# Optimization experiments

Measured on AMD Instinct MI355X. Metric: run time of the kernel, lower is better.

Reference implementation:

```python
import jax, jax.numpy as jnp
import numpy as np

N = 10000
E = 640000
D = 128
EPS = 1e-8


def _gcn_conv(x, src, dst, deg_isqrt, W, b, n):
    # PyG GCNConv: h = x @ W; out_i = sum_{j->i} (d_j^-1/2 d_i^-1/2) h_j; out += b
    h = x @ W                                   # [N, Dout]
    norm = deg_isqrt[src] * deg_isqrt[dst]      # [E']
    msgs = h[src] * norm[:, None]               # [E', Dout] gather
    out = jax.ops.segment_sum(msgs, dst, num_segments=n)  # scatter-add
    return out + b


def _pairnorm_pn(x):
    # mode 'PN': divide each row by its L2 norm
    norm = jnp.sqrt(jnp.sum(x * x, axis=1, keepdims=True)) + EPS
    return x / norm


def setup_inputs() -> dict:
    key = jax.random.key(0)
    ks = jax.random.split(key, 8)
    x = jax.random.normal(ks[0], (N, D), dtype=jnp.float32)
    edge_index = jax.random.randint(ks[1], (2, E), 0, N, dtype=jnp.int64)
    scale = 1.0 / np.sqrt(D)
    W1 = jax.random.normal(ks[2], (D, D), dtype=jnp.float32) * scale
    b1 = jnp.zeros((D,), dtype=jnp.float32)
    W2 = jax.random.normal(ks[3], (D, D), dtype=jnp.float32) * scale
    b2 = jnp.zeros((D,), dtype=jnp.float32)
    W3 = jax.random.normal(ks[4], (D, D), dtype=jnp.float32) * scale
    b3 = jnp.zeros((D,), dtype=jnp.float32)
    return {"x": x, "edge_index": edge_index, "W1": W1, "b1": b1,
            "W2": W2, "b2": b2, "W3": W3, "b3": b3}


def reference(x, edge_index, W1, b1, W2, b2, W3, b3):
    n = x.shape[0]
    loops = jnp.arange(n, dtype=edge_index.dtype)
    src = jnp.concatenate([edge_index[0], loops])  # add self loops
    dst = jnp.concatenate([edge_index[1], loops])
    deg = jax.ops.segment_sum(jnp.ones_like(dst, dtype=x.dtype), dst, num_segments=n)
    deg_isqrt = jnp.where(deg > 0, jax.lax.rsqrt(jnp.maximum(deg, 1.0)), 0.0)

    prev = x  # in_channels == hidden_channels -> identity skip
    for W, b in ((W1, b1), (W2, b2)):
        x = _gcn_conv(x, src, dst, deg_isqrt, W, b, n)
        x = _pairnorm_pn(x)
        x = x + prev
        prev = x
        x = jax.nn.gelu(x, approximate=False)  # torch F.gelu default = exact erf
        # dropout p=0.0 / eval: identity
    return _gcn_conv(x, src, dst, deg_isqrt, W3, b3, n)
```

## Files before the change

kernel.cpp:

```cpp
#include <hip/hip_runtime.h>
#include <hip/hip_bf16.h>
#include <hip/hip_fp16.h>
#include <math.h>

#define D 128
#define PAD 16
#define MAXDEG 192
#define WKROW 65

typedef _Float16 h2 __attribute__((ext_vector_type(2)));

__global__ void zero_strided(int* __restrict__ p, int n) {
    int i = blockIdx.x * blockDim.x + threadIdx.x;
    if (i < n) p[(size_t)i * PAD] = 0;
}

__global__ void csr_direct(const int* __restrict__ ei, int E,
                           int* __restrict__ cnt, unsigned short* __restrict__ slots) {
    int t = blockIdx.x * blockDim.x + threadIdx.x;
    int e0 = t * 2;
    if (e0 + 1 < E) {
        int2 s = *(const int2*)(ei + e0);
        int2 d = *(const int2*)(ei + E + e0);
        int p0 = atomicAdd(&cnt[(size_t)d.x * PAD], 1);
        int p1 = atomicAdd(&cnt[(size_t)d.y * PAD], 1);
        if (p0 < MAXDEG) __builtin_nontemporal_store((unsigned short)s.x, &slots[(size_t)d.x * MAXDEG + p0]);
        if (p1 < MAXDEG) __builtin_nontemporal_store((unsigned short)s.y, &slots[(size_t)d.y * MAXDEG + p1]);
    } else if (e0 < E) {
        int sv = ei[e0], dv = ei[E + e0];
        int p = atomicAdd(&cnt[(size_t)dv * PAD], 1);
        if (p < MAXDEG) __builtin_nontemporal_store((unsigned short)sv, &slots[(size_t)dv * MAXDEG + p]);
    }
}

__global__ void prep_kernel(const float* __restrict__ x, const int* __restrict__ cnt,
                            unsigned* __restrict__ xb, int n) {
    int t = blockIdx.x * blockDim.x + threadIdx.x;
    if (t < n * 64) {
        int i = t >> 6;
        float di = rsqrtf((float)(cnt[(size_t)i * PAD] + 1));
        float2 v = ((const float2*)x)[t];
        union { h2 h; unsigned u; } pk;
        pk.h = (h2){(_Float16)(di * v.x), (_Float16)(di * v.y)};
        xb[t] = pk.u;
    }
}

__device__ __forceinline__ h2 shxor_h2(h2 v, int m) {
    union { h2 h; int i; } a, b;
    a.h = v;
    b.i = __shfl_xor(a.i, m);
    return b.h;
}

union U4H { uint4 u; h2 h[4]; };

#define ACCH(U) do { ha0 += (U).h[0]; ha1 += (U).h[1]; ha2 += (U).h[2]; ha3 += (U).h[3]; } while (0)

__global__ __launch_bounds__(512, 8) void layer_kernel(
        const unsigned* __restrict__ xb,
        const int* __restrict__ cnt, const unsigned short* __restrict__ slots,
        const float* __restrict__ W, const float* __restrict__ bias,
        const float* __restrict__ prev, float* __restrict__ pout,
        unsigned* __restrict__ xbout, float* __restrict__ out3,
        int n, int mode, int wp) {
    __shared__ unsigned Wk[D * WKROW];
    __shared__ unsigned yh[8 * 64];
    {
        const float4* W4 = (const float4*)W;
#pragma unroll
        for (int it = 0; it < 4; ++it) {
            int t2 = it * 512 + threadIdx.x;
            int k2 = t2 >> 5, c4 = t2 & 31;
            float4 wa = W4[(2 * k2) * 32 + c4];
            float4 wb = W4[(2 * k2 + 1) * 32 + c4];
            int jb = c4 << 2;
            union { h2 h; unsigned u; } p0, p1, p2, p3;
            p0.h = (h2){(_Float16)wa.x, (_Float16)wb.x};
            p1.h = (h2){(_Float16)wa.y, (_Float16)wb.y};
            p2.h = (h2){(_Float16)wa.z, (_Float16)wb.z};
            p3.h = (h2){(_Float16)wa.w, (_Float16)wb.w};
            Wk[(jb + 0) * WKROW + k2] = p0.u;
            Wk[(jb + 1) * WKROW + k2] = p1.u;
            Wk[(jb + 2) * WKROW + k2] = p2.u;
            Wk[(jb + 3) * WKROW + k2] = p3.u;
        }
    }
    __syncthreads();

    int w = threadIdx.x >> 6, l = threadIdx.x & 63;
    int i = blockIdx.x * 8 + w;
    if (i >= n) return;
    int q = l >> 4, r = l & 15;
    const uint4* g4 = (const uint4*)xb;

    h2 ha0 = (h2){0, 0}, ha1 = (h2){0, 0}, ha2 = (h2){0, 0}, ha3 = (h2){0, 0};
    if (q == 0) {
        U4H s; s.u = g4[(size_t)i * 16 + r];
        ha0 = s.h[0]; ha1 = s.h[1]; ha2 = s.h[2]; ha3 = s.h[3];
    }

    int cc = cnt[(size_t)i * PAD];
    float di = rsqrtf((float)(cc + 1));
    int c = min(cc, MAXDEG);
    const unsigned short* row = slots + (size_t)i * MAXDEG;
    int e = 0;
    for (; e + 16 <= c; e += 16) {
        int s0 = row[e + q];
        int s1 = row[e + 4 + q];
        int s2 = row[e + 8 + q];
        int s3 = row[e + 12 + q];
        U4H u0, u1, u2, u3;
        u0.u = g4[(size_t)s0 * 16 + r];
        u1.u = g4[(size_t)s1 * 16 + r];
        u2.u = g4[(size_t)s2 * 16 + r];
        u3.u = g4[(size_t)s3 * 16 + r];
        ACCH(u0); ACCH(u1); ACCH(u2); ACCH(u3);
    }
    if (e + 8 <= c) {
        int s0 = row[e + q];
        int s1 = row[e + 4 + q];
        U4H u0, u1;
        u0.u = g4[(size_t)s0 * 16 + r];
        u1.u = g4[(size_t)s1 * 16 + r];
        ACCH(u0); ACCH(u1);
        e += 8;
    }
    if (e + 4 <= c) {
        U4H u0; u0.u = g4[(size_t)row[e + q] * 16 + r];
        ACCH(u0);
        e += 4;
    }
    int rem = c - e;
    if (q < rem) {
        U4H u0; u0.u = g4[(size_t)row[e + q] * 16 + r];
        ACCH(u0);
    }

    ha0 += shxor_h2(ha0, 16); ha0 += shxor_h2(ha0, 32);
    ha1 += shxor_h2(ha1, 16); ha1 += shxor_h2(ha1, 32);
    ha2 += shxor_h2(ha2, 16); ha2 += shxor_h2(ha2, 32);
    ha3 += shxor_h2(ha3, 16); ha3 += shxor_h2(ha3, 32);

    h2 hs = (q & 2) ? ((q & 1) ? ha3 : ha2) : ((q & 1) ? ha1 : ha0);
    int p = 4 * r + q;
    union { h2 h; unsigned u; } ys; ys.h = hs;
    yh[w * 64 + p] = ys.u;

    const unsigned* yrow = yh + w * 64;
    float t0 = 0.f, t1 = 0.f;
#pragma unroll 4
    for (int k2 = 0; k2 < 64; ++k2) {
        union { unsigned u; h2 h; } yk, w0, w1;
        yk.u = yrow[k2];
        w0.u = Wk[l * WKROW + k2];
        w1.u = Wk[(l + 64) * WKROW + k2];
        t0 = __builtin_amdgcn_fdot2(yk.h, w0.h, t0, false);
        t1 = __builtin_amdgcn_fdot2(yk.h, w1.h, t1, false);
    }
    float c0 = fmaf(di, t0, bias[l]);
    float c1 = fmaf(di, t1, bias[l + 64]);

    if (mode) {
        out3[(size_t)i * D + l]      = c0;
        out3[(size_t)i * D + l + 64] = c1;
        return;
    }

    float ss = c0 * c0 + c1 * c1;
#pragma unroll
    for (int m = 1; m < 64; m <<= 1) ss += __shfl_xor(ss, m);
    float inv = 1.0f / (sqrtf(ss) + 1e-8f);

    float p0 = fmaf(c0, inv, prev[(size_t)i * D + l]);
    float p1 = fmaf(c1, inv, prev[(size_t)i * D + l + 64]);
    if (wp) {
        pout[(size_t)i * D + l]      = p0;
        pout[(size_t)i * D + l + 64] = p1;
    }

    const float ISQ2 = 0.70710678118654752440f;
    float g0 = 0.5f * p0 * (1.0f + erff(p0 * ISQ2));
    float g1 = 0.5f * p1 * (1.0f + erff(p1 * ISQ2));
    _Float16* xo = (_Float16*)xbout;
    xo[(size_t)i * D + l]      = (_Float16)(di * g0);
    xo[(size_t)i * D + l + 64] = (_Float16)(di * g1);
}

extern "C" void kernel_launch(void* const* d_in, const int* in_sizes, int n_in,
                              void* d_out, int out_size, void* d_ws, size_t ws_size,
                              hipStream_t stream) {
    const float* x  = (const float*)d_in[0];
    const int*   ei = (const int*)d_in[1];
    const float* W1 = (const float*)d_in[2];
    const float* b1 = (const float*)d_in[3];
    const float* W2 = (const float*)d_in[4];
    const float* b2 = (const float*)d_in[5];
    const float* W3 = (const float*)d_in[6];
    const float* b3 = (const float*)d_in[7];
    int n = in_sizes[0] / D;
    int E = in_sizes[1] / 2;

    char* p = (char*)d_ws;
    auto carve = [&](size_t bytes) {
        char* q = p;
        p += (bytes + 511) & ~(size_t)511;
        return q;
    };
    int* cnt = (int*)carve((size_t)n * PAD * 4);
    unsigned short* slots = (unsigned short*)carve((size_t)n * MAXDEG * 2);
    unsigned* xb0 = (unsigned*)carve((size_t)n * D * 2);
    unsigned* xb1 = (unsigned*)carve((size_t)n * D * 2);
    float* pa  = (float*)d_out;
    float* out = (float*)d_out;

    zero_strided<<<(n + 255) / 256, 256, 0, stream>>>(cnt, n);
    csr_direct<<<((E + 1) / 2 + 255) / 256, 256, 0, stream>>>(ei, E, cnt, slots);
    prep_kernel<<<(n * 64 + 255) / 256, 256, 0, stream>>>(x, cnt, xb0, n);

    int lb = (n + 7) / 8;
    layer_kernel<<<lb, 512, 0, stream>>>(xb0, cnt, slots, W1, b1, x,  pa, xb1, nullptr, n, 0, 1);
    layer_kernel<<<lb, 512, 0, stream>>>(xb1, cnt, slots, W2, b2, pa, nullptr, xb0, nullptr, n, 0, 0);
    layer_kernel<<<lb, 512, 0, stream>>>(xb0, cnt, slots, W3, b3, nullptr, nullptr, nullptr, out, n, 1, 0);
}
```

Measured before the change: 111.4 us.

## Build CSR via two-pass bucket binning with shared-memory atomics

Replaces the per-edge global atomic CSR build with a two-pass scheme. The first pass bins edges into 64-node buckets using LDS counters and one global atomic per bucket per block. The second pass assembles each bucket's rows in shared memory and writes them out coalesced. This removes contended global atomics and scattered 2-byte stores, at the cost of an extra kernel, an intermediate bucket buffer, and a fixed bucket capacity that could overflow on skewed graphs.

```diff
diff --git a/kernel.cpp b/kernel.cpp
--- a/kernel.cpp
+++ b/kernel.cpp
@@ -4,32 +4,74 @@
 #include <math.h>
 
 #define D 128
-#define PAD 16
 #define MAXDEG 192
+#define BUK 64
+#define CAP 4608
 #define WKROW 65
 
 typedef _Float16 h2 __attribute__((ext_vector_type(2)));
 
-__global__ void zero_strided(int* __restrict__ p, int n) {
+__global__ void zero_ints(int* __restrict__ p, int m) {
     int i = blockIdx.x * blockDim.x + threadIdx.x;
-    if (i < n) p[(size_t)i * PAD] = 0;
-}
-
-__global__ void csr_direct(const int* __restrict__ ei, int E,
-                           int* __restrict__ cnt, unsigned short* __restrict__ slots) {
-    int t = blockIdx.x * blockDim.x + threadIdx.x;
-    int e0 = t * 2;
-    if (e0 + 1 < E) {
-        int2 s = *(const int2*)(ei + e0);
-        int2 d = *(const int2*)(ei + E + e0);
-        int p0 = atomicAdd(&cnt[(size_t)d.x * PAD], 1);
-        int p1 = atomicAdd(&cnt[(size_t)d.y * PAD], 1);
-        if (p0 < MAXDEG) __builtin_nontemporal_store((unsigned short)s.x, &slots[(size_t)d.x * MAXDEG + p0]);
-        if (p1 < MAXDEG) __builtin_nontemporal_store((unsigned short)s.y, &slots[(size_t)d.y * MAXDEG + p1]);
-    } else if (e0 < E) {
-        int sv = ei[e0], dv = ei[E + e0];
-        int p = atomicAdd(&cnt[(size_t)dv * PAD], 1);
-        if (p < MAXDEG) __builtin_nontemporal_store((unsigned short)sv, &slots[(size_t)dv * MAXDEG + p]);
+    if (i < m) p[i] = 0;
+}
+
+__global__ __launch_bounds__(256) void bin_kernel(const int* __restrict__ ei, int E,
+                                                  int nbuk, int* __restrict__ bcnt,
+                                                  unsigned* __restrict__ buckets) {
+    __shared__ int lcnt[256];
+    __shared__ int gbase[256];
+    int tid = threadIdx.x;
+    lcnt[tid] = 0;
+    __syncthreads();
+    int base = blockIdx.x * 2048;
+    int pk[8], lp[8], bk[8];
+#pragma unroll
+    for (int j = 0; j < 8; ++j) {
+        int e = base + j * 256 + tid;
+        if (e < E) {
+            int sv = ei[e], dv = ei[E + e];
+            bk[j] = dv >> 6;
+            pk[j] = (dv << 16) | sv;
+            lp[j] = atomicAdd(&lcnt[bk[j]], 1);
+        } else bk[j] = -1;
+    }
+    __syncthreads();
+    if (tid < nbuk) gbase[tid] = atomicAdd(&bcnt[tid], lcnt[tid]);
+    __syncthreads();
+#pragma unroll
+    for (int j = 0; j < 8; ++j) {
+        if (bk[j] >= 0) {
+            int pos = gbase[bk[j]] + lp[j];
+            if (pos < CAP) buckets[(size_t)bk[j] * CAP + pos] = (unsigned)pk[j];
+        }
+    }
+}
+
+__global__ __launch_bounds__(256) void csr_build(const int* __restrict__ bcnt,
+                                                 const unsigned* __restrict__ buckets,
+                                                 int n, int* __restrict__ cnt,
+                                                 unsigned short* __restrict__ slots) {
+    __shared__ unsigned short lrow[BUK * MAXDEG];
+    __shared__ int lcur[BUK];
+    int tid = threadIdx.x;
+    int b = blockIdx.x;
+    if (tid < BUK) lcur[tid] = 0;
+    __syncthreads();
+    int cb = min(bcnt[b], CAP);
+    for (int e = tid; e < cb; e += 256) {
+        unsigned u = buckets[(size_t)b * CAP + e];
+        int li = (int)(u >> 16) - b * BUK;
+        int pos = atomicAdd(&lcur[li], 1);
+        if (pos < MAXDEG) lrow[li * MAXDEG + pos] = (unsigned short)(u & 0xffffu);
+    }
+    __syncthreads();
+    unsigned* so = (unsigned*)slots + (size_t)b * (BUK * MAXDEG / 2);
+    const unsigned* lr = (const unsigned*)lrow;
+    for (int k = tid; k < BUK * MAXDEG / 2; k += 256) so[k] = lr[k];
+    if (tid < BUK) {
+        int node = b * BUK + tid;
+        if (node < n) cnt[node] = lcur[tid];
     }
 }
 
@@ -38,7 +80,7 @@
     int t = blockIdx.x * blockDim.x + threadIdx.x;
     if (t < n * 64) {
         int i = t >> 6;
-        float di = rsqrtf((float)(cnt[(size_t)i * PAD] + 1));
+        float di = rsqrtf((float)(cnt[i] + 1));
         float2 v = ((const float2*)x)[t];
         union { h2 h; unsigned u; } pk;
         pk.h = (h2){(_Float16)(di * v.x), (_Float16)(di * v.y)};
@@ -100,7 +142,7 @@
         ha0 = s.h[0]; ha1 = s.h[1]; ha2 = s.h[2]; ha3 = s.h[3];
     }
 
-    int cc = cnt[(size_t)i * PAD];
+    int cc = cnt[i];
     float di = rsqrtf((float)(cc + 1));
     int c = min(cc, MAXDEG);
     const unsigned short* row = slots + (size_t)i * MAXDEG;
@@ -158,22 +200,22 @@
         t0 = __builtin_amdgcn_fdot2(yk.h, w0.h, t0, false);
         t1 = __builtin_amdgcn_fdot2(yk.h, w1.h, t1, false);
     }
-    float c0 = fmaf(di, t0, bias[l]);
-    float c1 = fmaf(di, t1, bias[l + 64]);
+    float o0 = fmaf(di, t0, bias[l]);
+    float o1 = fmaf(di, t1, bias[l + 64]);
 
     if (mode) {
-        out3[(size_t)i * D + l]      = c0;
-        out3[(size_t)i * D + l + 64] = c1;
+        out3[(size_t)i * D + l]      = o0;
+        out3[(size_t)i * D + l + 64] = o1;
         return;
     }
 
-    float ss = c0 * c0 + c1 * c1;
+    float ss = o0 * o0 + o1 * o1;
 #pragma unroll
     for (int m = 1; m < 64; m <<= 1) ss += __shfl_xor(ss, m);
     float inv = 1.0f / (sqrtf(ss) + 1e-8f);
 
-    float p0 = fmaf(c0, inv, prev[(size_t)i * D + l]);
-    float p1 = fmaf(c1, inv, prev[(size_t)i * D + l + 64]);
+    float p0 = fmaf(o0, inv, prev[(size_t)i * D + l]);
+    float p1 = fmaf(o1, inv, prev[(size_t)i * D + l + 64]);
     if (wp) {
         pout[(size_t)i * D + l]      = p0;
         pout[(size_t)i * D + l + 64] = p1;
@@ -200,6 +242,7 @@
     const float* b3 = (const float*)d_in[7];
     int n = in_sizes[0] / D;
     int E = in_sizes[1] / 2;
+    int nbuk = (n + BUK - 1) / BUK;
 
     char* p = (char*)d_ws;
     auto carve = [&](size_t bytes) {
@@ -207,15 +250,18 @@
         p += (bytes + 511) & ~(size_t)511;
         return q;
     };
-    int* cnt = (int*)carve((size_t)n * PAD * 4);
-    unsigned short* slots = (unsigned short*)carve((size_t)n * MAXDEG * 2);
+    int* cnt = (int*)carve((size_t)n * 4);
+    int* bcnt = (int*)carve((size_t)nbuk * 4);
+    unsigned* buckets = (unsigned*)carve((size_t)nbuk * CAP * 4);
+    unsigned short* slots = (unsigned short*)carve((size_t)nbuk * BUK * MAXDEG * 2);
     unsigned* xb0 = (unsigned*)carve((size_t)n * D * 2);
     unsigned* xb1 = (unsigned*)carve((size_t)n * D * 2);
     float* pa  = (float*)d_out;
     float* out = (float*)d_out;
 
-    zero_strided<<<(n + 255) / 256, 256, 0, stream>>>(cnt, n);
-    csr_direct<<<((E + 1) / 2 + 255) / 256, 256, 0, stream>>>(ei, E, cnt, slots);
+    zero_ints<<<(nbuk + 255) / 256, 256, 0, stream>>>(bcnt, nbuk);
+    bin_kernel<<<(E + 2047) / 2048, 256, 0, stream>>>(ei, E, nbuk, bcnt, buckets);
+    csr_build<<<nbuk, 256, 0, stream>>>(bcnt, buckets, n, cnt, slots);
     prep_kernel<<<(n * 64 + 255) / 256, 256, 0, stream>>>(x, cnt, xb0, n);
 
     int lb = (n + 7) / 8;
```

Result: faster. 95.94 us (-13.9%).
